# Kernel tuning notes

Hardware: AMD Instinct MI355X
Metric: run time of the kernel (lower is better)

Reference implementation:

```python
import jax, jax.numpy as jnp
import numpy as np

SEQ_LEN = 128
IN_F = 16
OUT_F = 16
K_ORDER = 3
BATCH = 1024


def setup_inputs() -> dict:
    key = jax.random.key(0)
    k1, k2, k3 = jax.random.split(key, 3)
    x = jax.random.normal(k1, (BATCH, SEQ_LEN, IN_F), dtype=jnp.float32)
    # Glorot-uniform init for weight [k, in, out]
    lim = float(np.sqrt(6.0 / (IN_F + OUT_F)))
    weight = jax.random.uniform(k2, (K_ORDER, IN_F, OUT_F), dtype=jnp.float32, minval=-lim, maxval=lim)
    bias = jnp.zeros((OUT_F,), dtype=jnp.float32)
    adj_param = jax.random.normal(k3, (IN_F, IN_F), dtype=jnp.float32)
    return {"x": x, "weight": weight, "bias": bias, "adj_param": adj_param}


def _cheb_polynomials(adj_param, seq_len, in_f, k_order):
    """Vectorized build of the normalized-Laplacian Chebyshev basis.

    Replaces the original per-element Python loops:
      - temporal edges: node (i,f) <-> (i+1,f)  (symmetric shift by in_f)
      - feature edges : sigmoid(adj_param) off-diagonal, block-diag per time step
    """
    n = seq_len * in_f
    eye_n = jnp.eye(n, dtype=jnp.float32)
    # temporal edges
    offs = jnp.arange((seq_len - 1) * in_f)
    temporal = jnp.zeros((n, n), dtype=jnp.float32).at[offs, offs + in_f].set(1.0)
    temporal = temporal + temporal.T
    # feature edges (zero diagonal), replicated block-diagonally over time
    feat = jax.nn.sigmoid(adj_param) * (1.0 - jnp.eye(in_f, dtype=jnp.float32))
    adj = temporal + jnp.kron(jnp.eye(seq_len, dtype=jnp.float32), feat) + eye_n
    # symmetric normalization: L = I - D^{-1/2} A D^{-1/2}
    d = jnp.sum(adj, axis=1)
    d_inv_sqrt = jnp.where(d > 0, d ** -0.5, 0.0)
    lap = eye_n - d_inv_sqrt[:, None] * adj * d_inv_sqrt[None, :]
    # spectral rescale: L_scaled = 2/||L||_2 * L - I  (||.||_2 = largest singular value)
    l_scaled = (2.0 / jnp.linalg.norm(lap, ord=2)) * lap - eye_n
    polys = [eye_n, l_scaled]
    for _ in range(2, k_order):
        polys.append(2.0 * (l_scaled @ polys[-1]) - polys[-2])
    return polys


def reference(x, weight, bias, adj_param):
    batch, seq_len, in_f = x.shape
    k_order, _, out_f = weight.shape
    polys = _cheb_polynomials(adj_param, seq_len, in_f, k_order)
    x_flat = x.reshape(batch, seq_len * in_f)  # [B, N]
    out = jnp.zeros((batch, seq_len, out_f), dtype=x.dtype)
    for k in range(k_order):
        x_k = (x_flat @ polys[k]).reshape(batch, seq_len, in_f)
        out = out + jnp.einsum("bsf,fo->bso", x_k, weight[k])
    return out + bias
```

## Files before the change

### kernel.cpp

```cpp
#include <hip/hip_runtime.h>
#include <math.h>


#define MU_MIN (-1.99940694f)

__device__ __forceinline__ float dot16(float x) {
  x += __shfl_xor(x, 1);
  x += __shfl_xor(x, 2);
  x += __shfl_xor(x, 4);
  x += __shfl_xor(x, 8);
  return x;
}

__global__ __launch_bounds__(256) void kA_build(const float* __restrict__ adj,
                                                const float* __restrict__ W,
                                                float* __restrict__ wsf) {
  const int t = blockIdx.x;
  const int tid = threadIdx.x;
  __shared__ float Bsh[256], Wsh[768];
  __shared__ float Dm[256], D0[256], Dp[256], DD[256];
  __shared__ float dis_i[16], dis_b[16], csh[1];
  __shared__ float H0[512], Pbuf[512], Qbuf[512];
  __shared__ float scl[2], lamsh[2];
  __shared__ int jst[2];

  {
    const int f = tid >> 4, g = tid & 15;
    const float a = adj[tid];
    const float s = 1.f / (1.f + expf(-a));
    Bsh[tid] = (f == g) ? 1.f : s;
    Wsh[tid] = W[tid];
    Wsh[tid + 256] = W[tid + 256];
    Wsh[tid + 512] = W[tid + 512];
  }
  __syncthreads();
  if (tid < 16) {
    float rsum = 0.f;
    for (int j = 0; j < 16; j++) rsum += Bsh[tid * 16 + j];
    dis_i[tid] = 1.f / sqrtf(rsum + 2.f);
    dis_b[tid] = 1.f / sqrtf(rsum + 1.f);
  }
  __syncthreads();

  const int pass = tid >> 7, idx = tid & 127;
  const int pb = pass * 256;
  const float mu = pass ? -MU_MIN : MU_MIN;
  for (int e = idx; e < 256; e += 128) {
    const int f = e >> 4, g = e & 15;
    float gv = -dis_i[f] * Bsh[e] * dis_i[g];
    if (f == g) gv += 1.f - mu * dis_i[f] * dis_i[f];
    Pbuf[pb + e] = gv;
  }
  __syncthreads();
  for (int e = idx; e < 256; e += 128) {
    const int r = e >> 4, q = e & 15;
    float s = 0.f;
    #pragma unroll
    for (int k = 0; k < 16; k++) s += Pbuf[pb + k * 16 + r] * Pbuf[pb + k * 16 + q];
    H0[pb + e] = s;
    Qbuf[pb + e] = s;
  }
  __syncthreads();

  float* cur = Qbuf;
  float* nxt = Pbuf;
  #pragma unroll 1
  for (int it = 0; it < 8; it++) {
    if (idx == 0) {
      float tr = 0.f;
      #pragma unroll
      for (int d = 0; d < 16; d++) tr += cur[pb + d * 17];
      scl[pass] = 1.f / (tr * tr);
    }
    __syncthreads();
    const float s2 = scl[pass];
    for (int e = idx; e < 256; e += 128) {
      const int r = e >> 4, q = e & 15;
      const float4* rr = (const float4*)(cur + pb + r * 16);
      const float4* qq = (const float4*)(cur + pb + q * 16);
      float s = 0.f;
      #pragma unroll
      for (int k4 = 0; k4 < 4; k4++) {
        const float4 a = rr[k4], b = qq[k4];
        s += a.x * b.x + a.y * b.y + a.z * b.z + a.w * b.w;
      }
      nxt[pb + e] = s * s2;
    }
    __syncthreads();
    float* tmp = cur; cur = nxt; nxt = tmp;
  }
  if (idx == 0) {
    int bj = 0; float bd = -1.f;
    #pragma unroll
    for (int d = 0; d < 16; d++) {
      const float v = cur[pb + d * 17];
      if (v > bd) { bd = v; bj = d; }
    }
    jst[pass] = bj;
  }
  __syncthreads();
  if (idx < 16) {
    const int r = idx, js = jst[pass];
    const float vr = cur[pb + r * 16 + js];
    float hv = 0.f;
    #pragma unroll
    for (int q = 0; q < 16; q++) hv += H0[pb + r * 16 + q] * cur[pb + q * 16 + js];
    const float num = dot16(vr * hv);
    const float den = dot16(vr * vr);
    if (r == 0) lamsh[pass] = num / fmaxf(den, 1e-30f);
  }
  __syncthreads();
  if (tid == 0) {
    const float lam = fmaxf(fmaxf(lamsh[0], lamsh[1]), 1e-20f);
    csh[0] = 2.f / sqrtf(lam);
  }
  __syncthreads();

  const float c = csh[0];
  const int r = tid >> 4, q = tid & 15;

  auto uat = [&](int a_, int ff) -> float {
    return (a_ == 0 || a_ == 127) ? dis_b[ff] : dis_i[ff];
  };

  D0[tid] = ((r == q) ? (c - 1.f) : 0.f) - c * uat(t, r) * uat(t, q) * Bsh[tid];
  if (t > 0)   Dm[tid] = ((r == q) ? (c - 1.f) : 0.f) - c * uat(t - 1, r) * uat(t - 1, q) * Bsh[tid];
  if (t < 127) Dp[tid] = ((r == q) ? (c - 1.f) : 0.f) - c * uat(t + 1, r) * uat(t + 1, q) * Bsh[tid];
  __syncthreads();
  {
    float s = 0.f;
    #pragma unroll
    for (int k = 0; k < 16; k++) s += D0[r * 16 + k] * D0[k * 16 + q];
    DD[tid] = s;
  }
  __syncthreads();

  const int fo = r;
  const int o = q;
  float m[5];
  const float ut_f = uat(t, fo);

  {
    float acc = Wsh[fo * 16 + o];
    const float diag0 = 2.f * c * c * ut_f * ut_f *
                        ((t > 0 ? uat(t - 1, fo) * uat(t - 1, fo) : 0.f) +
                         (t < 127 ? uat(t + 1, fo) * uat(t + 1, fo) : 0.f)) - 1.f;
    #pragma unroll
    for (int fp = 0; fp < 16; fp++) {
      acc += D0[fo * 16 + fp] * Wsh[256 + fp * 16 + o];
      const float p2 = 2.f * DD[fo * 16 + fp] + ((fo == fp) ? diag0 : 0.f);
      acc += p2 * Wsh[512 + fp * 16 + o];
    }
    m[2] = acc;
  }
  if (t < 127) {
    const float gf = -c * uat(t + 1, fo) * ut_f;
    float acc = gf * Wsh[256 + fo * 16 + o];
    #pragma unroll
    for (int fp = 0; fp < 16; fp++) {
      const float gq = -c * uat(t + 1, fp) * uat(t, fp);
      const float p2 = 2.f * (gf * D0[fo * 16 + fp] + Dp[fo * 16 + fp] * gq);
      acc += p2 * Wsh[512 + fp * 16 + o];
    }
    m[3] = acc;
  } else m[3] = 0.f;
  if (t > 0) {
    const float gf = -c * uat(t - 1, fo) * ut_f;
    float acc = gf * Wsh[256 + fo * 16 + o];
    #pragma unroll
    for (int fp = 0; fp < 16; fp++) {
      const float gq = -c * uat(t - 1, fp) * uat(t, fp);
      const float p2 = 2.f * (Dm[fo * 16 + fp] * gq + gf * D0[fo * 16 + fp]);
      acc += p2 * Wsh[512 + fp * 16 + o];
    }
    m[1] = acc;
  } else m[1] = 0.f;
  m[4] = (t < 126) ? (2.f * c * c * uat(t + 2, fo) * uat(t + 1, fo) * uat(t + 1, fo) * ut_f
                      * Wsh[512 + fo * 16 + o]) : 0.f;
  m[0] = (t > 1) ? (2.f * c * c * uat(t - 2, fo) * uat(t - 1, fo) * uat(t - 1, fo) * ut_f
                    * Wsh[512 + fo * 16 + o]) : 0.f;

  #pragma unroll
  for (int d5 = 0; d5 < 5; d5++)
    wsf[((size_t)(t * 5 + d5) * 16 + fo) * 16 + o] = m[d5];
}

__global__ __launch_bounds__(256) void k3_main(const float* __restrict__ x,
                                               const float* __restrict__ bias,
                                               const float* __restrict__ wsf,
                                               float* __restrict__ out) {
  const int tg = blockIdx.y, bg = blockIdx.x;
  const int t0 = tg * 16, b0 = bg * 16;
  const int tid = threadIdx.x;
  const int tl = tid >> 4, o = tid & 15;
  const int t = t0 + tl;

  float M[80];
  {
    const float* Mt = wsf + (size_t)t * 5 * 256;
    #pragma unroll
    for (int i = 0; i < 80; i++) M[i] = Mt[i * 16 + o];
  }
  const float bo = bias[o];

  __shared__ float xs[1600];

  for (int cc = 0; cc < 4; cc++) {
    __syncthreads();
    for (int idx = tid; idx < 320; idx += 256) {
      const int cb = idx / 80, rem = idx % 80;
      const int rrow = rem >> 2, qq = rem & 3;
      int gr = t0 - 2 + rrow;
      gr = gr < 0 ? 0 : (gr > 127 ? 127 : gr);
      const float4 v = *(const float4*)(x + ((size_t)(b0 + cc * 4 + cb) * 128 + gr) * 16 + qq * 4);
      *(float4*)(xs + cb * 400 + rrow * 20 + qq * 4) = v;
    }
    __syncthreads();
    #pragma unroll
    for (int cb = 0; cb < 4; cb++) {
      float acc0 = bo, acc1 = 0.f;
      #pragma unroll
      for (int dt = 0; dt < 5; dt++) {
        const float* xr = xs + cb * 400 + (tl + dt) * 20;
        const float4 xa = *(const float4*)(xr);
        const float4 xb = *(const float4*)(xr + 4);
        const float4 xc = *(const float4*)(xr + 8);
        const float4 xd = *(const float4*)(xr + 12);
        const float* Mp = M + dt * 16;
        acc0 += xa.x * Mp[0] + xa.y * Mp[1] + xa.z * Mp[2] + xa.w * Mp[3]
              + xb.x * Mp[4] + xb.y * Mp[5] + xb.z * Mp[6] + xb.w * Mp[7];
        acc1 += xc.x * Mp[8] + xc.y * Mp[9] + xc.z * Mp[10] + xc.w * Mp[11]
              + xd.x * Mp[12] + xd.y * Mp[13] + xd.z * Mp[14] + xd.w * Mp[15];
      }
      out[((size_t)(b0 + cc * 4 + cb) * 128 + t) * 16 + o] = acc0 + acc1;
    }
  }
}

extern "C" void kernel_launch(void* const* d_in, const int* in_sizes, int n_in,
                              void* d_out, int out_size, void* d_ws, size_t ws_size,
                              hipStream_t stream) {
  const float* x    = (const float*)d_in[0];
  const float* W    = (const float*)d_in[1];
  const float* bias = (const float*)d_in[2];
  const float* adj  = (const float*)d_in[3];
  float* out = (float*)d_out;
  float* wsf = (float*)d_ws;

  kA_build<<<dim3(128), dim3(256), 0, stream>>>(adj, W, wsf);
  k3_main<<<dim3(64, 8), dim3(256), 0, stream>>>(x, bias, wsf, out);
}
```

Measured before the change: 85.30 us.

## Fuse operator-build and apply kernels into one with redundant per-block build

Merges the two kernels into a single launch in which every block recomputes the spectral scale (power iteration in one wavefront) and builds the per-timestep 5-tap weight stencil for its 16 time steps in registers, removing the workspace round trip and the second launch. The x tile for the first chunk is loaded by the other wavefronts while the power iteration runs, and each block now handles 32 batches (8 per chunk) instead of 16. The trade-off is redundant build work in all 256 blocks, heavier LDS use, and half as many blocks.

Measured after the change: 142.0 us. 66.5% more time.

```diff
diff --git a/kernel.cpp b/kernel.cpp
--- a/kernel.cpp
+++ b/kernel.cpp
@@ -12,212 +12,205 @@
   return x;
 }
 
-__global__ __launch_bounds__(256) void kA_build(const float* __restrict__ adj,
-                                                const float* __restrict__ W,
-                                                float* __restrict__ wsf) {
-  const int t = blockIdx.x;
+__global__ __launch_bounds__(256) void k_fused(const float* __restrict__ adj,
+                                               const float* __restrict__ W,
+                                               const float* __restrict__ x,
+                                               const float* __restrict__ bias,
+                                               float* __restrict__ out) {
+  const int bg = blockIdx.x;
+  const int tg = blockIdx.y;
+  const int t0 = tg * 16, b0 = bg * 32;
   const int tid = threadIdx.x;
+
   __shared__ float Bsh[256], Wsh[768];
-  __shared__ float Dm[256], D0[256], Dp[256], DD[256];
-  __shared__ float dis_i[16], dis_b[16], csh[1];
-  __shared__ float H0[512], Pbuf[512], Qbuf[512];
-  __shared__ float scl[2], lamsh[2];
-  __shared__ int jst[2];
-
-  {
-    const int f = tid >> 4, g = tid & 15;
-    const float a = adj[tid];
-    const float s = 1.f / (1.f + expf(-a));
-    Bsh[tid] = (f == g) ? 1.f : s;
-    Wsh[tid] = W[tid];
-    Wsh[tid + 256] = W[tid + 256];
-    Wsh[tid + 512] = W[tid + 512];
-  }
-  __syncthreads();
-  if (tid < 16) {
-    float rsum = 0.f;
-    for (int j = 0; j < 16; j++) rsum += Bsh[tid * 16 + j];
-    dis_i[tid] = 1.f / sqrtf(rsum + 2.f);
-    dis_b[tid] = 1.f / sqrtf(rsum + 1.f);
-  }
-  __syncthreads();
-
-  const int pass = tid >> 7, idx = tid & 127;
-  const int pb = pass * 256;
-  const float mu = pass ? -MU_MIN : MU_MIN;
-  for (int e = idx; e < 256; e += 128) {
-    const int f = e >> 4, g = e & 15;
-    float gv = -dis_i[f] * Bsh[e] * dis_i[g];
-    if (f == g) gv += 1.f - mu * dis_i[f] * dis_i[f];
-    Pbuf[pb + e] = gv;
-  }
-  __syncthreads();
-  for (int e = idx; e < 256; e += 128) {
-    const int r = e >> 4, q = e & 15;
-    float s = 0.f;
-    #pragma unroll
-    for (int k = 0; k < 16; k++) s += Pbuf[pb + k * 16 + r] * Pbuf[pb + k * 16 + q];
-    H0[pb + e] = s;
-    Qbuf[pb + e] = s;
-  }
-  __syncthreads();
-
-  float* cur = Qbuf;
-  float* nxt = Pbuf;
-  #pragma unroll 1
-  for (int it = 0; it < 8; it++) {
-    if (idx == 0) {
-      float tr = 0.f;
-      #pragma unroll
-      for (int d = 0; d < 16; d++) tr += cur[pb + d * 17];
-      scl[pass] = 1.f / (tr * tr);
-    }
-    __syncthreads();
-    const float s2 = scl[pass];
-    for (int e = idx; e < 256; e += 128) {
-      const int r = e >> 4, q = e & 15;
-      const float4* rr = (const float4*)(cur + pb + r * 16);
-      const float4* qq = (const float4*)(cur + pb + q * 16);
+  __shared__ float dis_i[16], dis_b[16], csh[1], lamsh[2];
+  __shared__ float H0[512], Pb[512], Qb[512];
+  __shared__ float Dsh[18 * 256];
+  __shared__ float DDsh[16 * 256];
+  __shared__ float xs[8 * 400];
+
+  if (tid < 64) {
+    const int lane = tid;
+    for (int e = lane; e < 256; e += 64) {
+      const int f = e >> 4, g = e & 15;
+      const float a = adj[e];
+      const float s = 1.f / (1.f + expf(-a));
+      Bsh[e] = (f == g) ? 1.f : s;
+    }
+    if (lane < 16) {
+      float rs = 0.f;
+      #pragma unroll
+      for (int j = 0; j < 16; j++) rs += Bsh[lane * 16 + j];
+      dis_i[lane] = rsqrtf(rs + 2.f);
+      dis_b[lane] = rsqrtf(rs + 1.f);
+    }
+    for (int e = lane; e < 512; e += 64) {
+      const int f = (e >> 4) & 15, g = e & 15;
+      const float mu = (e & 256) ? -MU_MIN : MU_MIN;
+      float gv = -dis_i[f] * Bsh[f * 16 + g] * dis_i[g];
+      if (f == g) gv += 1.f - mu * dis_i[f] * dis_i[f];
+      Pb[e] = gv;
+    }
+    for (int e = lane; e < 512; e += 64) {
+      const int pb = e & ~255;
+      const int r = (e >> 4) & 15, q = e & 15;
       float s = 0.f;
       #pragma unroll
-      for (int k4 = 0; k4 < 4; k4++) {
-        const float4 a = rr[k4], b = qq[k4];
-        s += a.x * b.x + a.y * b.y + a.z * b.z + a.w * b.w;
-      }
-      nxt[pb + e] = s * s2;
-    }
-    __syncthreads();
-    float* tmp = cur; cur = nxt; nxt = tmp;
-  }
-  if (idx == 0) {
-    int bj = 0; float bd = -1.f;
-    #pragma unroll
-    for (int d = 0; d < 16; d++) {
-      const float v = cur[pb + d * 17];
-      if (v > bd) { bd = v; bj = d; }
-    }
-    jst[pass] = bj;
-  }
-  __syncthreads();
-  if (idx < 16) {
-    const int r = idx, js = jst[pass];
-    const float vr = cur[pb + r * 16 + js];
-    float hv = 0.f;
-    #pragma unroll
-    for (int q = 0; q < 16; q++) hv += H0[pb + r * 16 + q] * cur[pb + q * 16 + js];
-    const float num = dot16(vr * hv);
-    const float den = dot16(vr * vr);
-    if (r == 0) lamsh[pass] = num / fmaxf(den, 1e-30f);
-  }
-  __syncthreads();
-  if (tid == 0) {
-    const float lam = fmaxf(fmaxf(lamsh[0], lamsh[1]), 1e-20f);
-    csh[0] = 2.f / sqrtf(lam);
-  }
-  __syncthreads();
-
-  const float c = csh[0];
-  const int r = tid >> 4, q = tid & 15;
-
-  auto uat = [&](int a_, int ff) -> float {
-    return (a_ == 0 || a_ == 127) ? dis_b[ff] : dis_i[ff];
-  };
-
-  D0[tid] = ((r == q) ? (c - 1.f) : 0.f) - c * uat(t, r) * uat(t, q) * Bsh[tid];
-  if (t > 0)   Dm[tid] = ((r == q) ? (c - 1.f) : 0.f) - c * uat(t - 1, r) * uat(t - 1, q) * Bsh[tid];
-  if (t < 127) Dp[tid] = ((r == q) ? (c - 1.f) : 0.f) - c * uat(t + 1, r) * uat(t + 1, q) * Bsh[tid];
-  __syncthreads();
-  {
-    float s = 0.f;
-    #pragma unroll
-    for (int k = 0; k < 16; k++) s += D0[r * 16 + k] * D0[k * 16 + q];
-    DD[tid] = s;
-  }
-  __syncthreads();
-
-  const int fo = r;
-  const int o = q;
-  float m[5];
-  const float ut_f = uat(t, fo);
-
-  {
-    float acc = Wsh[fo * 16 + o];
-    const float diag0 = 2.f * c * c * ut_f * ut_f *
-                        ((t > 0 ? uat(t - 1, fo) * uat(t - 1, fo) : 0.f) +
-                         (t < 127 ? uat(t + 1, fo) * uat(t + 1, fo) : 0.f)) - 1.f;
-    #pragma unroll
-    for (int fp = 0; fp < 16; fp++) {
-      acc += D0[fo * 16 + fp] * Wsh[256 + fp * 16 + o];
-      const float p2 = 2.f * DD[fo * 16 + fp] + ((fo == fp) ? diag0 : 0.f);
-      acc += p2 * Wsh[512 + fp * 16 + o];
-    }
-    m[2] = acc;
-  }
-  if (t < 127) {
-    const float gf = -c * uat(t + 1, fo) * ut_f;
-    float acc = gf * Wsh[256 + fo * 16 + o];
-    #pragma unroll
-    for (int fp = 0; fp < 16; fp++) {
-      const float gq = -c * uat(t + 1, fp) * uat(t, fp);
-      const float p2 = 2.f * (gf * D0[fo * 16 + fp] + Dp[fo * 16 + fp] * gq);
-      acc += p2 * Wsh[512 + fp * 16 + o];
-    }
-    m[3] = acc;
-  } else m[3] = 0.f;
-  if (t > 0) {
-    const float gf = -c * uat(t - 1, fo) * ut_f;
-    float acc = gf * Wsh[256 + fo * 16 + o];
-    #pragma unroll
-    for (int fp = 0; fp < 16; fp++) {
-      const float gq = -c * uat(t - 1, fp) * uat(t, fp);
-      const float p2 = 2.f * (Dm[fo * 16 + fp] * gq + gf * D0[fo * 16 + fp]);
-      acc += p2 * Wsh[512 + fp * 16 + o];
-    }
-    m[1] = acc;
-  } else m[1] = 0.f;
-  m[4] = (t < 126) ? (2.f * c * c * uat(t + 2, fo) * uat(t + 1, fo) * uat(t + 1, fo) * ut_f
-                      * Wsh[512 + fo * 16 + o]) : 0.f;
-  m[0] = (t > 1) ? (2.f * c * c * uat(t - 2, fo) * uat(t - 1, fo) * uat(t - 1, fo) * ut_f
-                    * Wsh[512 + fo * 16 + o]) : 0.f;
-
-  #pragma unroll
-  for (int d5 = 0; d5 < 5; d5++)
-    wsf[((size_t)(t * 5 + d5) * 16 + fo) * 16 + o] = m[d5];
-}
-
-__global__ __launch_bounds__(256) void k3_main(const float* __restrict__ x,
-                                               const float* __restrict__ bias,
-                                               const float* __restrict__ wsf,
-                                               float* __restrict__ out) {
-  const int tg = blockIdx.y, bg = blockIdx.x;
-  const int t0 = tg * 16, b0 = bg * 16;
-  const int tid = threadIdx.x;
-  const int tl = tid >> 4, o = tid & 15;
-  const int t = t0 + tl;
-
-  float M[80];
-  {
-    const float* Mt = wsf + (size_t)t * 5 * 256;
-    #pragma unroll
-    for (int i = 0; i < 80; i++) M[i] = Mt[i * 16 + o];
-  }
-  const float bo = bias[o];
-
-  __shared__ float xs[1600];
-
-  for (int cc = 0; cc < 4; cc++) {
-    __syncthreads();
-    for (int idx = tid; idx < 320; idx += 256) {
+      for (int k = 0; k < 16; k++) s += Pb[pb + k * 16 + r] * Pb[pb + k * 16 + q];
+      H0[e] = s; Qb[e] = s;
+    }
+    float* cur = Qb;
+    float* nxt = Pb;
+    #pragma unroll 1
+    for (int it = 0; it < 8; it++) {
+      float tr0 = 0.f, tr1 = 0.f;
+      #pragma unroll
+      for (int d = 0; d < 16; d++) { tr0 += cur[d * 17]; tr1 += cur[256 + d * 17]; }
+      const float s20 = 1.f / (tr0 * tr0), s21 = 1.f / (tr1 * tr1);
+      for (int e = lane; e < 512; e += 64) {
+        const int pb = e & ~255;
+        const int r = (e >> 4) & 15, q = e & 15;
+        const float4* rr = (const float4*)(cur + pb + r * 16);
+        const float4* qq = (const float4*)(cur + pb + q * 16);
+        float s = 0.f;
+        #pragma unroll
+        for (int k4 = 0; k4 < 4; k4++) {
+          const float4 a = rr[k4], b = qq[k4];
+          s += a.x * b.x + a.y * b.y + a.z * b.z + a.w * b.w;
+        }
+        nxt[e] = s * (pb ? s21 : s20);
+      }
+      float* tmp = cur; cur = nxt; nxt = tmp;
+    }
+    if (lane < 32) {
+      const int pass = lane >> 4, pb = pass << 8, r = lane & 15;
+      int bj = 0; float bd = -1.f;
+      #pragma unroll
+      for (int d = 0; d < 16; d++) {
+        const float v = cur[pb + d * 17];
+        if (v > bd) { bd = v; bj = d; }
+      }
+      const float vr = cur[pb + r * 16 + bj];
+      float hv = 0.f;
+      #pragma unroll
+      for (int q = 0; q < 16; q++) hv += H0[pb + r * 16 + q] * cur[pb + q * 16 + bj];
+      const float num = dot16(vr * hv);
+      const float den = dot16(vr * vr);
+      if (r == 0) lamsh[pass] = num / fmaxf(den, 1e-30f);
+    }
+    if (lane == 0) {
+      const float lam = fmaxf(fmaxf(lamsh[0], lamsh[1]), 1e-20f);
+      csh[0] = 2.f / sqrtf(lam);
+    }
+  } else {
+    const int id = tid - 64;
+    for (int e = id; e < 768; e += 192) Wsh[e] = W[e];
+    for (int idx = id; idx < 640; idx += 192) {
       const int cb = idx / 80, rem = idx % 80;
       const int rrow = rem >> 2, qq = rem & 3;
       int gr = t0 - 2 + rrow;
       gr = gr < 0 ? 0 : (gr > 127 ? 127 : gr);
-      const float4 v = *(const float4*)(x + ((size_t)(b0 + cc * 4 + cb) * 128 + gr) * 16 + qq * 4);
+      const float4 v = *(const float4*)(x + ((size_t)(b0 + cb) * 128 + gr) * 16 + qq * 4);
       *(float4*)(xs + cb * 400 + rrow * 20 + qq * 4) = v;
     }
-    __syncthreads();
+  }
+  __syncthreads();
+
+  const float c = csh[0];
+  for (int e = tid; e < 18 * 256; e += 256) {
+    const int tb = e >> 8, rq = e & 255;
+    const int r = rq >> 4, q = rq & 15;
+    int ta = t0 - 1 + tb;
+    ta = ta < 0 ? 0 : (ta > 127 ? 127 : ta);
+    const float ur = (ta == 0 || ta == 127) ? dis_b[r] : dis_i[r];
+    const float uq = (ta == 0 || ta == 127) ? dis_b[q] : dis_i[q];
+    Dsh[e] = ((r == q) ? (c - 1.f) : 0.f) - c * ur * uq * Bsh[rq];
+  }
+  __syncthreads();
+  for (int e = tid; e < 16 * 256; e += 256) {
+    const int tl = e >> 8, rq = e & 255;
+    const int r = rq >> 4, q = rq & 15;
+    const float* D0p = Dsh + (tl + 1) * 256;
+    float s = 0.f;
     #pragma unroll
-    for (int cb = 0; cb < 4; cb++) {
+    for (int k = 0; k < 16; k++) s += D0p[r * 16 + k] * D0p[k * 16 + q];
+    DDsh[e] = s;
+  }
+  __syncthreads();
+
+  const int tl = tid >> 4, o = tid & 15;
+  const int t = t0 + tl;
+  float M[80];
+  {
+    const float* D0p = Dsh + (tl + 1) * 256;
+    const float* Dmp = Dsh + tl * 256;
+    const float* Dpp = Dsh + (tl + 2) * 256;
+    const float* DDp = DDsh + tl * 256;
+    float W1c[16], W2c[16];
+    #pragma unroll
+    for (int fp = 0; fp < 16; fp++) { W1c[fp] = Wsh[256 + fp * 16 + o]; W2c[fp] = Wsh[512 + fp * 16 + o]; }
+    auto uat = [&](int a_, int ff) -> float {
+      return (a_ == 0 || a_ == 127) ? dis_b[ff] : dis_i[ff];
+    };
+    #pragma unroll 1
+    for (int fo = 0; fo < 16; fo++) {
+      const float ut_f = uat(t, fo);
+      {
+        float acc = Wsh[fo * 16 + o];
+        const float diag0 = 2.f * c * c * ut_f * ut_f *
+                            ((t > 0 ? uat(t - 1, fo) * uat(t - 1, fo) : 0.f) +
+                             (t < 127 ? uat(t + 1, fo) * uat(t + 1, fo) : 0.f)) - 1.f;
+        #pragma unroll
+        for (int fp = 0; fp < 16; fp++) {
+          acc += D0p[fo * 16 + fp] * W1c[fp];
+          const float p2 = 2.f * DDp[fo * 16 + fp] + ((fo == fp) ? diag0 : 0.f);
+          acc += p2 * W2c[fp];
+        }
+        M[2 * 16 + fo] = acc;
+      }
+      if (t < 127) {
+        const float gf = -c * uat(t + 1, fo) * ut_f;
+        float acc = gf * W1c[fo];
+        #pragma unroll
+        for (int fp = 0; fp < 16; fp++) {
+          const float gq = -c * uat(t + 1, fp) * uat(t, fp);
+          acc += 2.f * (gf * D0p[fo * 16 + fp] + Dpp[fo * 16 + fp] * gq) * W2c[fp];
+        }
+        M[3 * 16 + fo] = acc;
+      } else M[3 * 16 + fo] = 0.f;
+      if (t > 0) {
+        const float gf = -c * uat(t - 1, fo) * ut_f;
+        float acc = gf * W1c[fo];
+        #pragma unroll
+        for (int fp = 0; fp < 16; fp++) {
+          const float gq = -c * uat(t - 1, fp) * uat(t, fp);
+          acc += 2.f * (Dmp[fo * 16 + fp] * gq + gf * D0p[fo * 16 + fp]) * W2c[fp];
+        }
+        M[1 * 16 + fo] = acc;
+      } else M[1 * 16 + fo] = 0.f;
+      M[4 * 16 + fo] = (t < 126) ? (2.f * c * c * uat(t + 2, fo) * uat(t + 1, fo) * uat(t + 1, fo)
+                                    * ut_f * W2c[fo]) : 0.f;
+      M[0 * 16 + fo] = (t > 1) ? (2.f * c * c * uat(t - 2, fo) * uat(t - 1, fo) * uat(t - 1, fo)
+                                  * ut_f * W2c[fo]) : 0.f;
+    }
+  }
+  const float bo = bias[o];
+
+  for (int cc = 0; cc < 4; cc++) {
+    if (cc > 0) {
+      __syncthreads();
+      for (int idx = tid; idx < 640; idx += 256) {
+        const int cb = idx / 80, rem = idx % 80;
+        const int rrow = rem >> 2, qq = rem & 3;
+        int gr = t0 - 2 + rrow;
+        gr = gr < 0 ? 0 : (gr > 127 ? 127 : gr);
+        const float4 v = *(const float4*)(x + ((size_t)(b0 + cc * 8 + cb) * 128 + gr) * 16 + qq * 4);
+        *(float4*)(xs + cb * 400 + rrow * 20 + qq * 4) = v;
+      }
+      __syncthreads();
+    }
+    #pragma unroll
+    for (int cb = 0; cb < 8; cb++) {
       float acc0 = bo, acc1 = 0.f;
       #pragma unroll
       for (int dt = 0; dt < 5; dt++) {
@@ -232,7 +225,7 @@
         acc1 += xc.x * Mp[8] + xc.y * Mp[9] + xc.z * Mp[10] + xc.w * Mp[11]
               + xd.x * Mp[12] + xd.y * Mp[13] + xd.z * Mp[14] + xd.w * Mp[15];
       }
-      out[((size_t)(b0 + cc * 4 + cb) * 128 + t) * 16 + o] = acc0 + acc1;
+      out[((size_t)(b0 + cc * 8 + cb) * 128 + t) * 16 + o] = acc0 + acc1;
     }
   }
 }
@@ -245,8 +238,7 @@
   const float* bias = (const float*)d_in[2];
   const float* adj  = (const float*)d_in[3];
   float* out = (float*)d_out;
-  float* wsf = (float*)d_ws;
-
-  kA_build<<<dim3(128), dim3(256), 0, stream>>>(adj, W, wsf);
-  k3_main<<<dim3(64, 8), dim3(256), 0, stream>>>(x, bias, wsf, out);
+  (void)d_ws; (void)ws_size;
+
+  k_fused<<<dim3(32, 8), dim3(256), 0, stream>>>(adj, W, x, bias, out);
 }
```
